# Kernel tuning notes

Measured on AMD Instinct MI355X. Metric: run time of the kernel, lower is better.

Reference implementation:

```python
import jax, jax.numpy as jnp
import numpy as np

H = 512

def setup_inputs() -> dict:
    key = jax.random.key(0)
    k1, k2, k3 = jax.random.split(key, 3)
    encoder_outputs = jax.random.normal(k1, (32, 4096, H), dtype=jnp.float32)  # (B,T,H)
    W = jax.random.normal(k2, (H, H), dtype=jnp.float32) * (1.0 / np.sqrt(H))  # attn.weight
    v = jax.random.normal(k3, (H,), dtype=jnp.float32) * (1.0 / np.sqrt(H))    # v param
    return {"encoder_outputs": encoder_outputs, "W": W, "v": v}

def reference(encoder_outputs, W, v):
    # score: energy = tanh(x @ W.T); attn_energies = v . energy over H -> (B,T)
    energy = jnp.tanh(jnp.einsum('bth,gh->btg', encoder_outputs, W))
    attn_energies = jnp.einsum('btg,g->bt', energy, v)
    # method == 'bmm': softmax over T, weighted sum over T -> (B,H)
    attn_w = jax.nn.softmax(attn_energies, axis=-1)
    out = jnp.einsum('bt,bth->bh', attn_w, encoder_outputs)
    return out
```

## Files before the change

### kernel.cpp

```cpp
#include <hip/hip_runtime.h>
#include <hip/hip_bf16.h>

typedef __attribute__((ext_vector_type(8))) short short8;
typedef __attribute__((ext_vector_type(4))) float f32x4;

#define B_SZ 32
#define T_SZ 4096
#define H_SZ 512
#define NROWS (B_SZ * T_SZ)

static __device__ __forceinline__ unsigned int pack2(float a, float b) {
  unsigned int r;
  asm("v_cvt_pk_bf16_f32 %0, %1, %2" : "=v"(r) : "v"(a), "v"(b));
  return r;
}

static __device__ __forceinline__ float fast_tanh(float x) {
  float e = __expf(2.0f * x);
  return 1.0f - 2.0f / (e + 1.0f);
}

__global__ __launch_bounds__(256) void prep_w_kernel(
    const float* __restrict__ W, uint4* __restrict__ Wfrag) {
  int s = blockIdx.x * 256 + threadIdx.x;
  int grow  = s >> 6;
  int kt    = (s >> 2) & 15;
  int kslot = s & 3;
  const float4* Wf4 = reinterpret_cast<const float4*>(W);
  float4 lo = Wf4[grow * 128 + kt * 8 + kslot * 2];
  float4 hi = Wf4[grow * 128 + kt * 8 + kslot * 2 + 1];
  uint4 u;
  u.x = pack2(lo.x, lo.y); u.y = pack2(lo.z, lo.w);
  u.z = pack2(hi.x, hi.y); u.w = pack2(hi.z, hi.w);
  int nb = grow >> 4, g = grow & 15;
  Wfrag[nb * 1024 + kt * 64 + kslot * 16 + g] = u;
}

__global__ __launch_bounds__(512, 4) void score_kernel(
    const float* __restrict__ X, const uint4* __restrict__ Wfrag,
    const float* __restrict__ v, float* __restrict__ scores) {
  __shared__ unsigned char WsB[2][16384];

  const int tid   = threadIdx.x;
  const int lane  = tid & 63;
  const int wave  = tid >> 6;
  const int frow  = lane & 15;
  const int kslot = lane >> 4;
  const size_t rowbase = (size_t)blockIdx.x * 128;
  const size_t arow = rowbase + wave * 16 + frow;

  #define STAGE(c, b)                                                           \
    {                                                                           \
      const char* src = (const char*)Wfrag + (size_t)(c) * 16384 +              \
                        wave * 2048 + lane * 16;                                \
      unsigned char* dst = &WsB[b][wave * 2048];                                \
      _Pragma("unroll")                                                         \
      for (int i = 0; i < 2; ++i)                                               \
        __builtin_amdgcn_global_load_lds((const unsigned int*)(src + i * 1024), \
                                         (unsigned int*)(dst + i * 1024), 16, 0, 0); \
    }

  STAGE(0, 0);

  short8 afrag[16];
  {
    const float4* xr = reinterpret_cast<const float4*>(X + arow * H_SZ);
    #pragma unroll
    for (int kt = 0; kt < 16; ++kt) {
      float4 lo = xr[kt * 8 + kslot * 2];
      float4 hi = xr[kt * 8 + kslot * 2 + 1];
      union { uint4 u; short8 s; } cv;
      cv.u.x = pack2(lo.x, lo.y); cv.u.y = pack2(lo.z, lo.w);
      cv.u.z = pack2(hi.x, hi.y); cv.u.w = pack2(hi.z, hi.w);
      afrag[kt] = cv.s;
    }
  }
  __syncthreads();

  float red[4] = {0.f, 0.f, 0.f, 0.f};

  for (int ch = 0; ch < 32; ++ch) {
    if (ch < 31) STAGE(ch + 1, (ch + 1) & 1);
    float vg = v[ch * 16 + frow];

    f32x4 acc0 = {0.f, 0.f, 0.f, 0.f};
    f32x4 acc1 = {0.f, 0.f, 0.f, 0.f};
    const unsigned char* bb = &WsB[ch & 1][lane * 16];
    #pragma unroll
    for (int kt = 0; kt < 16; kt += 2) {
      short8 b0 = *reinterpret_cast<const short8*>(bb + kt * 1024);
      short8 b1 = *reinterpret_cast<const short8*>(bb + (kt + 1) * 1024);
      acc0 = __builtin_amdgcn_mfma_f32_16x16x32_bf16(afrag[kt],     b0, acc0, 0, 0, 0);
      acc1 = __builtin_amdgcn_mfma_f32_16x16x32_bf16(afrag[kt + 1], b1, acc1, 0, 0, 0);
    }
    #pragma unroll
    for (int r = 0; r < 4; ++r)
      red[r] = fmaf(vg, fast_tanh(acc0[r] + acc1[r]), red[r]);

    __syncthreads();
  }
  #undef STAGE

  #pragma unroll
  for (int r = 0; r < 4; ++r) {
    #pragma unroll
    for (int d = 1; d < 16; d <<= 1)
      red[r] += __shfl_xor(red[r], d);
  }
  if (frow == 0) {
    float* sp = scores + rowbase + wave * 16 + kslot * 4;
    sp[0] = red[0]; sp[1] = red[1]; sp[2] = red[2]; sp[3] = red[3];
  }
}

__global__ __launch_bounds__(256) void softmax_kernel(
    float* __restrict__ scores, float* __restrict__ denom) {
  const int b = blockIdx.x;
  float* s = scores + b * T_SZ;
  const int tid = threadIdx.x;
  __shared__ float redm[4], reds[4];

  float m = -1e30f;
  for (int t = tid; t < T_SZ; t += 256) m = fmaxf(m, s[t]);
  #pragma unroll
  for (int d = 1; d < 64; d <<= 1) m = fmaxf(m, __shfl_xor(m, d));
  if ((tid & 63) == 0) redm[tid >> 6] = m;
  __syncthreads();
  m = fmaxf(fmaxf(redm[0], redm[1]), fmaxf(redm[2], redm[3]));

  float sum = 0.f;
  for (int t = tid; t < T_SZ; t += 256) {
    float u = __expf(s[t] - m);
    s[t] = u;
    sum += u;
  }
  #pragma unroll
  for (int d = 1; d < 64; d <<= 1) sum += __shfl_xor(sum, d);
  if ((tid & 63) == 0) reds[tid >> 6] = sum;
  __syncthreads();
  if (tid == 0) denom[b] = reds[0] + reds[1] + reds[2] + reds[3];
}

__global__ __launch_bounds__(256) void wsum_kernel(
    const float* __restrict__ X, const float* __restrict__ u,
    float* __restrict__ partial) {
  const int ch = blockIdx.x;
  const int b  = blockIdx.y;
  const float* xb = X + ((size_t)b * T_SZ + ch * 128) * H_SZ;
  const float* ub = u + b * T_SZ + ch * 128;
  const int h2 = threadIdx.x;
  float ax = 0.f, ay = 0.f;
  for (int tt = 0; tt < 128; ++tt) {
    float w = ub[tt];
    float2 xv = reinterpret_cast<const float2*>(xb + (size_t)tt * H_SZ)[h2];
    ax = fmaf(w, xv.x, ax);
    ay = fmaf(w, xv.y, ay);
  }
  float2 r; r.x = ax; r.y = ay;
  reinterpret_cast<float2*>(partial + ((size_t)b * 32 + ch) * H_SZ)[h2] = r;
}

__global__ __launch_bounds__(256) void finalize_kernel(
    const float* __restrict__ partial, const float* __restrict__ denom,
    float* __restrict__ out) {
  const int b = blockIdx.x;
  const float inv = 1.0f / denom[b];
  for (int h = threadIdx.x; h < H_SZ; h += 256) {
    float s = 0.f;
    #pragma unroll
    for (int c = 0; c < 32; ++c) s += partial[((size_t)b * 32 + c) * H_SZ + h];
    out[b * H_SZ + h] = s * inv;
  }
}

extern "C" void kernel_launch(void* const* d_in, const int* in_sizes, int n_in,
                              void* d_out, int out_size, void* d_ws, size_t ws_size,
                              hipStream_t stream) {
  const float* X = (const float*)d_in[0];
  const float* W = (const float*)d_in[1];
  const float* v = (const float*)d_in[2];
  float* out = (float*)d_out;
  unsigned char* ws = (unsigned char*)d_ws;

  uint4* Wfrag   = (uint4*)(ws);
  float* scores  = (float*)(ws + (512u << 10));
  float* denom   = (float*)(ws + (1024u << 10));
  float* partial = (float*)(ws + (1024u << 10) + 512);

  prep_w_kernel<<<128, 256, 0, stream>>>(W, Wfrag);
  score_kernel<<<NROWS / 128, 512, 0, stream>>>(X, Wfrag, v, scores);
  softmax_kernel<<<B_SZ, 256, 0, stream>>>(scores, denom);
  dim3 g(32, B_SZ);
  wsum_kernel<<<g, 256, 0, stream>>>(X, scores, partial);
  finalize_kernel<<<B_SZ, 256, 0, stream>>>(partial, denom, out);
}
```

Measured before the change: 165.1 us.

## Fuse softmax and weighted sum into score kernel using online-softmax partials

Each score block now computes a local max and exp-sum over its 128 rows and, while those rows of X are likely still cache-resident, accumulates the weighted sum of X for them. A small combine kernel then rescales the 32 per-chunk partials per batch into the final output. This removes the separate softmax and wsum passes, including the second full read of X (256MB) and two kernel launches. In exchange the score kernel gains extra syncs and a strided per-column X re-read loop at the end.

After: 154.1 us. -6.7%, faster.

```diff
diff --git a/kernel.cpp b/kernel.cpp
--- a/kernel.cpp
+++ b/kernel.cpp
@@ -36,10 +36,14 @@
   Wfrag[nb * 1024 + kt * 64 + kslot * 16 + g] = u;
 }
 
-__global__ __launch_bounds__(512, 4) void score_kernel(
+__global__ __launch_bounds__(512, 4) void score_fused_kernel(
     const float* __restrict__ X, const uint4* __restrict__ Wfrag,
-    const float* __restrict__ v, float* __restrict__ scores) {
+    const float* __restrict__ v,
+    float* __restrict__ num, float2* __restrict__ md) {
   __shared__ unsigned char WsB[2][16384];
+  __shared__ float sLDS[128];
+  __shared__ float pLDS[128];
+  __shared__ float mred[2], dred[2];
 
   const int tid   = threadIdx.x;
   const int lane  = tid & 63;
@@ -80,8 +84,8 @@
   float red[4] = {0.f, 0.f, 0.f, 0.f};
 
   for (int ch = 0; ch < 32; ++ch) {
+    float vg = v[ch * 16 + frow];
     if (ch < 31) STAGE(ch + 1, (ch + 1) & 1);
-    float vg = v[ch * 16 + frow];
 
     f32x4 acc0 = {0.f, 0.f, 0.f, 0.f};
     f32x4 acc1 = {0.f, 0.f, 0.f, 0.f};
@@ -108,69 +112,58 @@
       red[r] += __shfl_xor(red[r], d);
   }
   if (frow == 0) {
-    float* sp = scores + rowbase + wave * 16 + kslot * 4;
+    float* sp = sLDS + wave * 16 + kslot * 4;
     sp[0] = red[0]; sp[1] = red[1]; sp[2] = red[2]; sp[3] = red[3];
+  }
+  __syncthreads();
+
+  if (tid < 128) {
+    float s = sLDS[tid];
+    float m = s;
+    #pragma unroll
+    for (int d = 1; d < 64; d <<= 1) m = fmaxf(m, __shfl_xor(m, d));
+    if ((tid & 63) == 0) mred[tid >> 6] = m;
+  }
+  __syncthreads();
+  const float m_loc = fmaxf(mred[0], mred[1]);
+  if (tid < 128) {
+    float p = __expf(sLDS[tid] - m_loc);
+    pLDS[tid] = p;
+    #pragma unroll
+    for (int d = 1; d < 64; d <<= 1) p += __shfl_xor(p, d);
+    if ((tid & 63) == 0) dred[tid >> 6] = p;
+  }
+  __syncthreads();
+
+  float a = 0.f;
+  const float* xb = X + rowbase * H_SZ + tid;
+  #pragma unroll 8
+  for (int t = 0; t < 128; ++t)
+    a = fmaf(pLDS[t], xb[(size_t)t * H_SZ], a);
+  num[(size_t)blockIdx.x * H_SZ + tid] = a;
+  if (tid == 0) {
+    float2 r; r.x = m_loc; r.y = dred[0] + dred[1];
+    md[blockIdx.x] = r;
   }
 }
 
-__global__ __launch_bounds__(256) void softmax_kernel(
-    float* __restrict__ scores, float* __restrict__ denom) {
-  const int b = blockIdx.x;
-  float* s = scores + b * T_SZ;
-  const int tid = threadIdx.x;
-  __shared__ float redm[4], reds[4];
-
-  float m = -1e30f;
-  for (int t = tid; t < T_SZ; t += 256) m = fmaxf(m, s[t]);
-  #pragma unroll
-  for (int d = 1; d < 64; d <<= 1) m = fmaxf(m, __shfl_xor(m, d));
-  if ((tid & 63) == 0) redm[tid >> 6] = m;
-  __syncthreads();
-  m = fmaxf(fmaxf(redm[0], redm[1]), fmaxf(redm[2], redm[3]));
-
-  float sum = 0.f;
-  for (int t = tid; t < T_SZ; t += 256) {
-    float u = __expf(s[t] - m);
-    s[t] = u;
-    sum += u;
-  }
-  #pragma unroll
-  for (int d = 1; d < 64; d <<= 1) sum += __shfl_xor(sum, d);
-  if ((tid & 63) == 0) reds[tid >> 6] = sum;
-  __syncthreads();
-  if (tid == 0) denom[b] = reds[0] + reds[1] + reds[2] + reds[3];
-}
-
-__global__ __launch_bounds__(256) void wsum_kernel(
-    const float* __restrict__ X, const float* __restrict__ u,
-    float* __restrict__ partial) {
-  const int ch = blockIdx.x;
-  const int b  = blockIdx.y;
-  const float* xb = X + ((size_t)b * T_SZ + ch * 128) * H_SZ;
-  const float* ub = u + b * T_SZ + ch * 128;
-  const int h2 = threadIdx.x;
-  float ax = 0.f, ay = 0.f;
-  for (int tt = 0; tt < 128; ++tt) {
-    float w = ub[tt];
-    float2 xv = reinterpret_cast<const float2*>(xb + (size_t)tt * H_SZ)[h2];
-    ax = fmaf(w, xv.x, ax);
-    ay = fmaf(w, xv.y, ay);
-  }
-  float2 r; r.x = ax; r.y = ay;
-  reinterpret_cast<float2*>(partial + ((size_t)b * 32 + ch) * H_SZ)[h2] = r;
-}
-
-__global__ __launch_bounds__(256) void finalize_kernel(
-    const float* __restrict__ partial, const float* __restrict__ denom,
+__global__ __launch_bounds__(512) void combine_kernel(
+    const float* __restrict__ num, const float2* __restrict__ md,
     float* __restrict__ out) {
   const int b = blockIdx.x;
-  const float inv = 1.0f / denom[b];
-  for (int h = threadIdx.x; h < H_SZ; h += 256) {
-    float s = 0.f;
-    #pragma unroll
-    for (int c = 0; c < 32; ++c) s += partial[((size_t)b * 32 + c) * H_SZ + h];
-    out[b * H_SZ + h] = s * inv;
+  const int h = threadIdx.x;
+  float M = -1e30f;
+  #pragma unroll
+  for (int c = 0; c < 32; ++c) M = fmaxf(M, md[b * 32 + c].x);
+  float den = 0.f, acc = 0.f;
+  #pragma unroll 4
+  for (int c = 0; c < 32; ++c) {
+    float2 m2 = md[b * 32 + c];
+    float w = __expf(m2.x - M);
+    den += w * m2.y;
+    acc = fmaf(w, num[(size_t)(b * 32 + c) * H_SZ + h], acc);
   }
+  out[b * H_SZ + h] = acc / den;
 }
 
 extern "C" void kernel_launch(void* const* d_in, const int* in_sizes, int n_in,
@@ -182,15 +175,11 @@
   float* out = (float*)d_out;
   unsigned char* ws = (unsigned char*)d_ws;
 
-  uint4* Wfrag   = (uint4*)(ws);
-  float* scores  = (float*)(ws + (512u << 10));
-  float* denom   = (float*)(ws + (1024u << 10));
-  float* partial = (float*)(ws + (1024u << 10) + 512);
+  uint4* Wfrag = (uint4*)(ws);
+  float* num   = (float*)(ws + (512u << 10));
+  float2* md   = (float2*)(ws + (512u << 10) + (2u << 20));
 
   prep_w_kernel<<<128, 256, 0, stream>>>(W, Wfrag);
-  score_kernel<<<NROWS / 128, 512, 0, stream>>>(X, Wfrag, v, scores);
-  softmax_kernel<<<B_SZ, 256, 0, stream>>>(scores, denom);
-  dim3 g(32, B_SZ);
-  wsum_kernel<<<g, 256, 0, stream>>>(X, scores, partial);
-  finalize_kernel<<<B_SZ, 256, 0, stream>>>(partial, denom, out);
+  score_fused_kernel<<<NROWS / 128, 512, 0, stream>>>(X, Wfrag, v, num, md);
+  combine_kernel<<<B_SZ, 512, 0, stream>>>(num, md, out);
 }
```
